# Kernel optimization log

Hardware: AMD Instinct MI355X
Metric: run time of the kernel (lower is better)

Reference implementation:

```python
import jax, jax.numpy as jnp
import numpy as np

N = 50000      # nodes
E = 800000     # edges
DIN = 128      # input feature dim
H = 128        # hidden_channels (cfg.gnn.dim_inner)
DOUT = 64      # output classes
EPS = 1e-5


def setup_inputs() -> dict:
    key = jax.random.key(0)
    ks = jax.random.split(key, 24)
    w = lambda k, s: jax.random.normal(k, s, jnp.float32) * 0.05
    return {
        "x": jax.random.normal(ks[0], (N, DIN), jnp.float32),
        "edge_index": jax.random.randint(ks[1], (2, E), 0, N, jnp.int32),
        # pre-processing 2-layer MLP
        "pre_w1": w(ks[2], (DIN, H)), "pre_b1": jnp.zeros((H,), jnp.float32),
        "pre_w2": w(ks[3], (H, H)),   "pre_b2": jnp.zeros((H,), jnp.float32),
        # 3 GCNConv layers
        "conv_w0": w(ks[4], (H, H)), "conv_b0": jnp.zeros((H,), jnp.float32),
        "conv_w1": w(ks[5], (H, H)), "conv_b1": jnp.zeros((H,), jnp.float32),
        "conv_w2": w(ks[6], (H, H)), "conv_b2": jnp.zeros((H,), jnp.float32),
        # BatchNorm affine params (after conv0 and conv1)
        "bn_g0": jnp.ones((H,), jnp.float32), "bn_b0": jnp.zeros((H,), jnp.float32),
        "bn_g1": jnp.ones((H,), jnp.float32), "bn_b1": jnp.zeros((H,), jnp.float32),
        # post-processing 2-layer MLP
        "post_w1": w(ks[7], (H, H)),    "post_b1": jnp.zeros((H,), jnp.float32),
        "post_w2": w(ks[8], (H, DOUT)), "post_b2": jnp.zeros((DOUT,), jnp.float32),
    }


def _gcn_norm(edge_index):
    # add self loops, compute symmetric normalization D^-1/2 A D^-1/2
    loops = jnp.arange(N, dtype=edge_index.dtype)
    src = jnp.concatenate([edge_index[0], loops])  # [E+N]
    dst = jnp.concatenate([edge_index[1], loops])
    deg = jax.ops.segment_sum(jnp.ones_like(src, jnp.float32), dst, num_segments=N)
    dinv = jnp.where(deg > 0, jax.lax.rsqrt(deg), 0.0)
    norm = dinv[src] * dinv[dst]                   # [E+N]
    return src, dst, norm


def _gcn_conv(x, W, b, src, dst, norm):
    h = x @ W                                      # [N, F_out]
    msg = h[src] * norm[:, None]                   # gather + scale  [E+N, F_out]
    return jax.ops.segment_sum(msg, dst, num_segments=N) + b


def _bn(x, g, b):
    m = x.mean(axis=0)
    v = x.var(axis=0)  # biased, as torch BN uses for normalization
    return (x - m) * jax.lax.rsqrt(v + EPS) * g + b


def reference(x, edge_index, pre_w1, pre_b1, pre_w2, pre_b2,
              conv_w0, conv_b0, conv_w1, conv_b1, conv_w2, conv_b2,
              bn_g0, bn_b0, bn_g1, bn_b1,
              post_w1, post_b1, post_w2, post_b2):
    src, dst, norm = _gcn_norm(edge_index)
    # pre-proc MLP (dropout=0)
    h = jax.nn.relu(x @ pre_w1 + pre_b1)
    h = jax.nn.relu(h @ pre_w2 + pre_b2)
    # conv -> BN -> relu (x2), then final conv
    h = jax.nn.relu(_bn(_gcn_conv(h, conv_w0, conv_b0, src, dst, norm), bn_g0, bn_b0))
    h = jax.nn.relu(_bn(_gcn_conv(h, conv_w1, conv_b1, src, dst, norm), bn_g1, bn_b1))
    h = _gcn_conv(h, conv_w2, conv_b2, src, dst, norm)
    # post-proc MLP
    h = jax.nn.relu(h @ post_w1 + post_b1)
    return h @ post_w2 + post_b2  # [N, DOUT] node logits
```

## Files before the change

kernel.cpp:

```cpp
#include <hip/hip_runtime.h>
#include <hip/hip_bf16.h>

#define NN 50000
#define EE 800000
#define DIN 128
#define HH 128
#define DOUT 64
#define BN_EPS 1e-5f

typedef __attribute__((ext_vector_type(8))) short short8;
typedef __attribute__((ext_vector_type(4))) float floatx4;

static inline size_t align_up(size_t x, size_t a) { return (x + a - 1) & ~(a - 1); }

__device__ __forceinline__ float bf2f(ushort u) {
    uint v = ((uint)u) << 16;
    return __builtin_bit_cast(float, v);
}
__device__ __forceinline__ float bf2f_lo(uint u) { return __builtin_bit_cast(float, u << 16); }
__device__ __forceinline__ float bf2f_hi(uint u) { return __builtin_bit_cast(float, u & 0xffff0000u); }
__device__ __forceinline__ ushort f2bf(float f) {
    uint u = __builtin_bit_cast(uint, f);
    u += 0x7fff + ((u >> 16) & 1);
    return (ushort)(u >> 16);
}
__device__ __forceinline__ uint pack_bf2(float lo, float hi) {
    return (uint)f2bf(lo) | ((uint)f2bf(hi) << 16);
}

__global__ void tcast_all_kernel(const float* __restrict__ s0, const float* __restrict__ s1,
                                 const float* __restrict__ s2, const float* __restrict__ s3,
                                 const float* __restrict__ s4, const float* __restrict__ s5,
                                 const float* __restrict__ s6,
                                 ushort* __restrict__ d0, ushort* __restrict__ d1,
                                 ushort* __restrict__ d2, ushort* __restrict__ d3,
                                 ushort* __restrict__ d4, ushort* __restrict__ d5,
                                 ushort* __restrict__ d6) {
    const float* src; ushort* dst; int F = 128;
    switch (blockIdx.y) {
        case 0: src = s0; dst = d0; break;
        case 1: src = s1; dst = d1; break;
        case 2: src = s2; dst = d2; break;
        case 3: src = s3; dst = d3; break;
        case 4: src = s4; dst = d4; break;
        case 5: src = s5; dst = d5; break;
        default: src = s6; dst = d6; F = 64; break;
    }
    int t = blockIdx.x * 256 + threadIdx.x;
    if (t >= F * 128) return;
    int f = t >> 7, k = t & 127;
    dst[t] = f2bf(src[(size_t)k * F + f]);
}

__global__ void cnt_kernel(const int* __restrict__ ei, int* __restrict__ cnt, int E) {
    int e = (blockIdx.x * 256 + threadIdx.x) * 4;
    if (e + 3 < E) {
        int4 d = *(const int4*)(ei + E + e);
        atomicAdd(&cnt[d.x], 1);
        atomicAdd(&cnt[d.y], 1);
        atomicAdd(&cnt[d.z], 1);
        atomicAdd(&cnt[d.w], 1);
    } else {
        for (; e < E; ++e) atomicAdd(&cnt[ei[E + e]], 1);
    }
}

__device__ __forceinline__ void block_scan256(int v, int* lsum, int& excl, int& total) {
    int lane = threadIdx.x & 63, w = threadIdx.x >> 6;
    int inc = v;
    #pragma unroll
    for (int s = 1; s < 64; s <<= 1) {
        int t = __shfl_up(inc, s);
        if (lane >= s) inc += t;
    }
    if (lane == 63) lsum[w] = inc;
    __syncthreads();
    int pre = 0;
    #pragma unroll
    for (int k = 0; k < 4; ++k)
        if (k < w) pre += lsum[k];
    excl = pre + inc - v;
    total = lsum[0] + lsum[1] + lsum[2] + lsum[3];
    __syncthreads();
}

__global__ void scan_part_kernel(const int* __restrict__ cnt, int* __restrict__ off,
                                 int* __restrict__ bsum, float* __restrict__ dinv, int n) {
    __shared__ int lsum[4];
    int i = blockIdx.x * 256 + threadIdx.x;
    int v = (i < n) ? cnt[i] : 0;
    int excl, total;
    block_scan256(v, lsum, excl, total);
    if (i < n) {
        off[i] = excl;
        dinv[i] = rsqrtf((float)(v + 1));
    }
    if (threadIdx.x == 0) bsum[blockIdx.x] = total;
}

__global__ void scan_bsum_kernel(int* __restrict__ bsum, int nb) {
    __shared__ int lsum[4];
    int t = threadIdx.x;
    int v = (t < nb) ? bsum[t] : 0;
    int excl, total;
    block_scan256(v, lsum, excl, total);
    if (t < nb) bsum[t] = excl;
}

__global__ void scan_add_kernel(int* __restrict__ off, const int* __restrict__ bsum,
                                int* __restrict__ cursor, int n) {
    int i = blockIdx.x * 256 + threadIdx.x;
    if (i < n) {
        int v = off[i] + bsum[blockIdx.x];
        off[i] = v;
        cursor[i] = v;
    }
    if (i == 0) off[n] = EE;
}

__global__ void fill_kernel(const int* __restrict__ ei, int* __restrict__ cursor,
                            int2* __restrict__ csr, const float* __restrict__ dinv, int E) {
    int e = blockIdx.x * 256 + threadIdx.x;
    if (e < E) {
        int s = ei[e];
        int d = ei[E + e];
        int pos = atomicAdd(&cursor[d], 1);
        float w = dinv[s] * dinv[d];
        csr[pos] = make_int2(s, __builtin_bit_cast(int, w));
    }
}

template <int NCG>
__device__ __forceinline__ void zero_acc(floatx4 (&acc)[2][NCG]) {
    #pragma unroll
    for (int rg = 0; rg < 2; ++rg)
        #pragma unroll
        for (int cg = 0; cg < NCG; ++cg)
            acc[rg][cg] = (floatx4){0.f, 0.f, 0.f, 0.f};
}

template <int FO>
__device__ __forceinline__ void stage_w(const ushort* __restrict__ Wt, uint4* Wl, int tid) {
    #pragma unroll
    for (int c = tid; c < FO * 16; c += 256) {
        int f = c >> 4, kb = c & 15;
        Wl[f * 16 + (kb ^ (f & 15))] = ((const uint4*)Wt)[c];
    }
}

template <int NCG>
__device__ __forceinline__ void gemm_step(const uint4* Xl, const uint4* Wl,
                                          floatx4 (&acc)[2][NCG], int wv, int lr, int lk) {
    #pragma unroll
    for (int ks = 0; ks < 4; ++ks) {
        int kb = ks * 4 + lk;
        int swz = kb ^ lr;
        short8 a0 = *(const short8*)&Xl[(wv * 32 + lr) * 16 + swz];
        short8 a1 = *(const short8*)&Xl[(wv * 32 + 16 + lr) * 16 + swz];
        #pragma unroll
        for (int cg = 0; cg < NCG; ++cg) {
            short8 b = *(const short8*)&Wl[(cg * 16 + lr) * 16 + swz];
            acc[0][cg] = __builtin_amdgcn_mfma_f32_16x16x32_bf16(a0, b, acc[0][cg], 0, 0, 0);
            acc[1][cg] = __builtin_amdgcn_mfma_f32_16x16x32_bf16(a1, b, acc[1][cg], 0, 0, 0);
        }
    }
}

template <int NCG>
__device__ __forceinline__ void write_h(floatx4 (&acc)[2][NCG], uint4* Xl,
                                        const float* __restrict__ bias,
                                        int wv, int lr, int lk) {
    ushort* Xs = (ushort*)Xl;
    #pragma unroll
    for (int rg = 0; rg < 2; ++rg)
        #pragma unroll
        for (int cg = 0; cg < NCG; ++cg) {
            int col = cg * 16 + lr;
            float bv = bias[col];
            #pragma unroll
            for (int j = 0; j < 4; ++j) {
                int row = wv * 32 + rg * 16 + lk * 4 + j;
                float o = fmaxf(acc[rg][cg][j] + bv, 0.f);
                Xs[(row * 16 + ((col >> 3) ^ (row & 15))) * 8 + (col & 7)] = f2bf(o);
            }
        }
}

template <int FOUT, bool RELU, bool BIAS, bool OUTF32>
__device__ __forceinline__ void epilogue(floatx4 (&acc)[2][FOUT / 16],
                                         const float* __restrict__ bias, void* Yout,
                                         int row0, int n, int wv, int lr, int lk) {
    #pragma unroll
    for (int rg = 0; rg < 2; ++rg) {
        int rbase = row0 + wv * 32 + rg * 16 + lk * 4;
        #pragma unroll
        for (int cg = 0; cg < FOUT / 16; ++cg) {
            int col = cg * 16 + lr;
            float bv = BIAS ? bias[col] : 0.f;
            #pragma unroll
            for (int j = 0; j < 4; ++j) {
                int r = rbase + j;
                if (r < n) {
                    float o = acc[rg][cg][j] + bv;
                    if (RELU) o = fmaxf(o, 0.f);
                    if (OUTF32)
                        ((float*)Yout)[(size_t)r * FOUT + col] = o;
                    else
                        ((ushort*)Yout)[(size_t)r * FOUT + col] = f2bf(o);
                }
            }
        }
    }
}

__global__ __launch_bounds__(256, 2) void fused_pre_kernel(
    const float* __restrict__ Xg, const ushort* __restrict__ W1t, const float* __restrict__ b1,
    const ushort* __restrict__ W2t, const float* __restrict__ b2,
    const ushort* __restrict__ W3t, ushort* __restrict__ Yout, int n) {
    __shared__ uint4 lds4[4096];
    uint4* Xl = lds4;
    uint4* Wl = lds4 + 2048;
    const int tid = threadIdx.x;
    const int row0 = blockIdx.x * 128;

    for (int c = tid; c < 2048; c += 256) {
        int r = c >> 4, kb = c & 15;
        int row = row0 + r;
        uint4 v = make_uint4(0, 0, 0, 0);
        if (row < n) {
            const float4* p = (const float4*)(Xg + (size_t)row * 128 + kb * 8);
            float4 x0 = p[0], x1 = p[1];
            v.x = pack_bf2(x0.x, x0.y);
            v.y = pack_bf2(x0.z, x0.w);
            v.z = pack_bf2(x1.x, x1.y);
            v.w = pack_bf2(x1.z, x1.w);
        }
        Xl[r * 16 + (kb ^ (r & 15))] = v;
    }
    stage_w<128>(W1t, Wl, tid);
    __syncthreads();

    const int wv = tid >> 6, lane = tid & 63;
    const int lr = lane & 15, lk = lane >> 4;

    floatx4 acc[2][8];
    zero_acc<8>(acc);
    gemm_step<8>(Xl, Wl, acc, wv, lr, lk);
    __syncthreads();
    write_h<8>(acc, Xl, b1, wv, lr, lk);
    stage_w<128>(W2t, Wl, tid);
    __syncthreads();

    zero_acc<8>(acc);
    gemm_step<8>(Xl, Wl, acc, wv, lr, lk);
    __syncthreads();
    write_h<8>(acc, Xl, b2, wv, lr, lk);
    stage_w<128>(W3t, Wl, tid);
    __syncthreads();

    zero_acc<8>(acc);
    gemm_step<8>(Xl, Wl, acc, wv, lr, lk);
    epilogue<128, false, false, false>(acc, nullptr, Yout, row0, n, wv, lr, lk);
}

__global__ __launch_bounds__(256, 2) void fused_post_kernel(
    const ushort* __restrict__ Xg, const ushort* __restrict__ W1t, const float* __restrict__ b1,
    const ushort* __restrict__ W2t, const float* __restrict__ b2,
    float* __restrict__ Yout, int n) {
    __shared__ uint4 lds4[4096];
    uint4* Xl = lds4;
    uint4* Wl = lds4 + 2048;
    const int tid = threadIdx.x;
    const int row0 = blockIdx.x * 128;

    for (int c = tid; c < 2048; c += 256) {
        int r = c >> 4, kb = c & 15;
        int row = row0 + r;
        uint4 v = make_uint4(0, 0, 0, 0);
        if (row < n) v = ((const uint4*)(Xg + (size_t)row * 128))[kb];
        Xl[r * 16 + (kb ^ (r & 15))] = v;
    }
    stage_w<128>(W1t, Wl, tid);
    __syncthreads();

    const int wv = tid >> 6, lane = tid & 63;
    const int lr = lane & 15, lk = lane >> 4;

    floatx4 acc[2][8];
    zero_acc<8>(acc);
    gemm_step<8>(Xl, Wl, acc, wv, lr, lk);
    __syncthreads();
    write_h<8>(acc, Xl, b1, wv, lr, lk);
    stage_w<64>(W2t, Wl, tid);
    __syncthreads();

    floatx4 acc2[2][4];
    zero_acc<4>(acc2);
    gemm_step<4>(Xl, Wl, acc2, wv, lr, lk);
    epilogue<64, false, true, true>(acc2, b2, Yout, row0, n, wv, lr, lk);
}

__global__ __launch_bounds__(256, 2) void gemm_bnf_kernel(
    const ushort* __restrict__ Xg, const ushort* __restrict__ Wt,
    const float* __restrict__ sums, const float* __restrict__ sumsq,
    const float* __restrict__ g, const float* __restrict__ bb,
    ushort* __restrict__ Yout, int n) {
    __shared__ uint4 lds4[4096];
    __shared__ float scf[128], shf[128];
    uint4* Xl = lds4;
    uint4* Wl = lds4 + 2048;
    const int tid = threadIdx.x;
    const int row0 = blockIdx.x * 128;

    if (tid < 128) {
        const float inv_n = 1.0f / (float)NN;
        float m = sums[tid] * inv_n;
        float var = sumsq[tid] * inv_n - m * m;
        float sc = g[tid] * rsqrtf(var + BN_EPS);
        scf[tid] = sc;
        shf[tid] = bb[tid] - m * sc;
    }
    stage_w<128>(Wt, Wl, tid);
    __syncthreads();

    for (int c = tid; c < 2048; c += 256) {
        int r = c >> 4, kb = c & 15;
        int row = row0 + r;
        uint4 v = make_uint4(0, 0, 0, 0);
        if (row < n) v = ((const uint4*)(Xg + (size_t)row * 128))[kb];
        uint a[4] = {v.x, v.y, v.z, v.w};
        #pragma unroll
        for (int p = 0; p < 4; ++p) {
            int f0 = kb * 8 + p * 2;
            float lo = fmaxf(fmaf(bf2f_lo(a[p]), scf[f0], shf[f0]), 0.f);
            float hi = fmaxf(fmaf(bf2f_hi(a[p]), scf[f0 + 1], shf[f0 + 1]), 0.f);
            a[p] = pack_bf2(lo, hi);
        }
        Xl[r * 16 + (kb ^ (r & 15))] = make_uint4(a[0], a[1], a[2], a[3]);
    }
    __syncthreads();

    const int wv = tid >> 6, lane = tid & 63;
    const int lr = lane & 15, lk = lane >> 4;

    floatx4 acc[2][8];
    zero_acc<8>(acc);
    gemm_step<8>(Xl, Wl, acc, wv, lr, lk);
    epilogue<128, false, false, false>(acc, nullptr, Yout, row0, n, wv, lr, lk);
}

__global__ __launch_bounds__(256) void agg16_kernel(const ushort* __restrict__ h,
                                                    const float* __restrict__ dinv,
                                                    const int* __restrict__ off,
                                                    const int2* __restrict__ csr,
                                                    const float* __restrict__ bias,
                                                    ushort* __restrict__ out, int n) {
    int i = (blockIdx.x * 256 + threadIdx.x) >> 6;
    if (i >= n) return;
    int lane = threadIdx.x & 63;

    float di = dinv[i];
    float sw = di * di;
    uint u = ((const uint*)(h + (size_t)i * 128))[lane];
    float a0 = bf2f_lo(u) * sw, a1 = bf2f_hi(u) * sw;

    const int s0 = off[i], s1 = off[i + 1];
    int j = s0;
    for (; j + 4 <= s1; j += 4) {
        int2 ea = csr[j + 0], eb = csr[j + 1];
        int2 ec = csr[j + 2], ed = csr[j + 3];
        float wa = __builtin_bit_cast(float, ea.y), wb = __builtin_bit_cast(float, eb.y);
        float wc = __builtin_bit_cast(float, ec.y), wd = __builtin_bit_cast(float, ed.y);
        uint ua = ((const uint*)(h + (size_t)ea.x * 128))[lane];
        uint ub = ((const uint*)(h + (size_t)eb.x * 128))[lane];
        uint uc = ((const uint*)(h + (size_t)ec.x * 128))[lane];
        uint ud = ((const uint*)(h + (size_t)ed.x * 128))[lane];
        a0 += bf2f_lo(ua) * wa + bf2f_lo(ub) * wb + bf2f_lo(uc) * wc + bf2f_lo(ud) * wd;
        a1 += bf2f_hi(ua) * wa + bf2f_hi(ub) * wb + bf2f_hi(uc) * wc + bf2f_hi(ud) * wd;
    }
    for (; j < s1; ++j) {
        int2 e = csr[j];
        float w = __builtin_bit_cast(float, e.y);
        uint uv = ((const uint*)(h + (size_t)e.x * 128))[lane];
        a0 += bf2f_lo(uv) * w;
        a1 += bf2f_hi(uv) * w;
    }

    float2 b2 = ((const float2*)bias)[lane];
    a0 += b2.x; a1 += b2.y;
    ((uint*)(out + (size_t)i * 128))[lane] = pack_bf2(a0, a1);
}

__global__ __launch_bounds__(256) void bn_stats16_kernel(const ushort* __restrict__ x,
                                                         float* __restrict__ sums,
                                                         float* __restrict__ sumsq, int n) {
    __shared__ float ls[128], lq[128];
    int tid = threadIdx.x;
    if (tid < 128) { ls[tid] = 0.f; lq[tid] = 0.f; }
    __syncthreads();
    int fg = tid & 15, rg = tid >> 4;
    float s[8] = {}, q[8] = {};
    for (int r = blockIdx.x * 16 + rg; r < n; r += gridDim.x * 16) {
        uint4 v = ((const uint4*)(x + (size_t)r * 128))[fg];
        uint a[4] = {v.x, v.y, v.z, v.w};
        #pragma unroll
        for (int p = 0; p < 4; ++p) {
            float lo = bf2f_lo(a[p]), hi = bf2f_hi(a[p]);
            s[2 * p] += lo;     q[2 * p] += lo * lo;
            s[2 * p + 1] += hi; q[2 * p + 1] += hi * hi;
        }
    }
    #pragma unroll
    for (int k = 0; k < 8; ++k) {
        atomicAdd(&ls[fg * 8 + k], s[k]);
        atomicAdd(&lq[fg * 8 + k], q[k]);
    }
    __syncthreads();
    if (tid < 128) {
        atomicAdd(&sums[tid], ls[tid]);
        atomicAdd(&sumsq[tid], lq[tid]);
    }
}

extern "C" void kernel_launch(void* const* d_in, const int* in_sizes, int n_in,
                              void* d_out, int out_size, void* d_ws, size_t ws_size,
                              hipStream_t stream) {
    const float* x        = (const float*)d_in[0];
    const int*   ei       = (const int*)d_in[1];
    const float* pre_w1   = (const float*)d_in[2];
    const float* pre_b1   = (const float*)d_in[3];
    const float* pre_w2   = (const float*)d_in[4];
    const float* pre_b2   = (const float*)d_in[5];
    const float* conv_w0  = (const float*)d_in[6];
    const float* conv_b0  = (const float*)d_in[7];
    const float* conv_w1  = (const float*)d_in[8];
    const float* conv_b1  = (const float*)d_in[9];
    const float* conv_w2  = (const float*)d_in[10];
    const float* conv_b2  = (const float*)d_in[11];
    const float* bn_g0    = (const float*)d_in[12];
    const float* bn_b0    = (const float*)d_in[13];
    const float* bn_g1    = (const float*)d_in[14];
    const float* bn_b1    = (const float*)d_in[15];
    const float* post_w1  = (const float*)d_in[16];
    const float* post_b1  = (const float*)d_in[17];
    const float* post_w2  = (const float*)d_in[18];
    const float* post_b2  = (const float*)d_in[19];
    float* out = (float*)d_out;

    const int n = NN, E = EE;
    const int NB = (n + 255) / 256;

    char* w = (char*)d_ws;
    int* cnt    = (int*)w;   w += (size_t)n * 4;
    float* bns0 = (float*)w;
    float* bnq0 = bns0 + 128;
    float* bns1 = bns0 + 256;
    float* bnq1 = bns0 + 384;
    w += align_up(512 * 4, 512);
    int* cursor = (int*)w;   w += align_up((size_t)n * 4, 512);
    int* bsum   = (int*)w;   w += align_up(256 * 4, 512);
    int* off    = (int*)w;   w += align_up((size_t)(n + 1) * 4, 512);
    float* dinv = (float*)w; w += align_up((size_t)n * 4, 512);
    int2* csr   = (int2*)w;  w += align_up((size_t)E * 8, 512);
    ushort* wt_pre1  = (ushort*)w; w += align_up(128 * 128 * 2, 512);
    ushort* wt_pre2  = (ushort*)w; w += align_up(128 * 128 * 2, 512);
    ushort* wt_c0    = (ushort*)w; w += align_up(128 * 128 * 2, 512);
    ushort* wt_c1    = (ushort*)w; w += align_up(128 * 128 * 2, 512);
    ushort* wt_c2    = (ushort*)w; w += align_up(128 * 128 * 2, 512);
    ushort* wt_post1 = (ushort*)w; w += align_up(128 * 128 * 2, 512);
    ushort* wt_post2 = (ushort*)w; w += align_up(64 * 128 * 2, 512);
    ushort* P = (ushort*)w; w += align_up((size_t)n * 128 * 2, 512);
    ushort* Q = (ushort*)w; w += align_up((size_t)n * 128 * 2, 512);
    ushort* R = (ushort*)w; w += align_up((size_t)n * 128 * 2, 512);

    hipMemsetAsync(cnt, 0, (size_t)n * 4 + 512 * 4, stream);

    tcast_all_kernel<<<dim3(64, 7), 256, 0, stream>>>(
        pre_w1, pre_w2, conv_w0, conv_w1, conv_w2, post_w1, post_w2,
        wt_pre1, wt_pre2, wt_c0, wt_c1, wt_c2, wt_post1, wt_post2);

    cnt_kernel<<<(E / 4 + 255) / 256, 256, 0, stream>>>(ei, cnt, E);
    scan_part_kernel<<<NB, 256, 0, stream>>>(cnt, off, bsum, dinv, n);
    scan_bsum_kernel<<<1, 256, 0, stream>>>(bsum, NB);
    scan_add_kernel<<<NB, 256, 0, stream>>>(off, bsum, cursor, n);
    fill_kernel<<<(E + 255) / 256, 256, 0, stream>>>(ei, cursor, csr, dinv, E);

    const int gb = (n + 127) / 128;
    const int agg_blocks = (n * 64 + 255) / 256;

    fused_pre_kernel<<<gb, 256, 0, stream>>>(x, wt_pre1, pre_b1, wt_pre2, pre_b2, wt_c0, P, n);
    agg16_kernel<<<agg_blocks, 256, 0, stream>>>(P, dinv, off, csr, conv_b0, Q, n);
    bn_stats16_kernel<<<256, 256, 0, stream>>>(Q, bns0, bnq0, n);

    gemm_bnf_kernel<<<gb, 256, 0, stream>>>(Q, wt_c1, bns0, bnq0, bn_g0, bn_b0, P, n);
    agg16_kernel<<<agg_blocks, 256, 0, stream>>>(P, dinv, off, csr, conv_b1, R, n);
    bn_stats16_kernel<<<256, 256, 0, stream>>>(R, bns1, bnq1, n);

    gemm_bnf_kernel<<<gb, 256, 0, stream>>>(R, wt_c2, bns1, bnq1, bn_g1, bn_b1, P, n);
    agg16_kernel<<<agg_blocks, 256, 0, stream>>>(P, dinv, off, csr, conv_b2, Q, n);

    fused_post_kernel<<<gb, 256, 0, stream>>>(Q, wt_post1, post_b1, wt_post2, post_b2, out, n);
}
```

Before: 408.8 us.

## Split GCN aggregation into feature quarters and store only source indices in CSR

The aggregation kernel now splits the 128 features into four 32-feature quarters, each handled by a separate block range. Within a quarter, each 16-lane group processes one node, and all blocks for a quarter are scheduled together. The aim is to keep that quarter's slice of the feature table resident in L2/LLC while the random neighbor gathers run. The CSR now stores only the source index, shrinking it from 8 to 4 bytes per edge; the edge weight is recomputed as dinv[src]*dinv[dst] inside the kernel. In exchange, each edge's index is read four times and needs an extra random dinv gather, and each gather fetches only 64 bytes per row.

```diff
diff --git a/kernel.cpp b/kernel.cpp
--- a/kernel.cpp
+++ b/kernel.cpp
@@ -119,14 +119,13 @@
 }
 
 __global__ void fill_kernel(const int* __restrict__ ei, int* __restrict__ cursor,
-                            int2* __restrict__ csr, const float* __restrict__ dinv, int E) {
+                            int* __restrict__ csr, int E) {
     int e = blockIdx.x * 256 + threadIdx.x;
     if (e < E) {
         int s = ei[e];
         int d = ei[E + e];
         int pos = atomicAdd(&cursor[d], 1);
-        float w = dinv[s] * dinv[d];
-        csr[pos] = make_int2(s, __builtin_bit_cast(int, w));
+        csr[pos] = s;
     }
 }
 
@@ -349,46 +348,52 @@
     epilogue<128, false, false, false>(acc, nullptr, Yout, row0, n, wv, lr, lk);
 }
 
-__global__ __launch_bounds__(256) void agg16_kernel(const ushort* __restrict__ h,
-                                                    const float* __restrict__ dinv,
-                                                    const int* __restrict__ off,
-                                                    const int2* __restrict__ csr,
-                                                    const float* __restrict__ bias,
-                                                    ushort* __restrict__ out, int n) {
-    int i = (blockIdx.x * 256 + threadIdx.x) >> 6;
-    if (i >= n) return;
-    int lane = threadIdx.x & 63;
-
-    float di = dinv[i];
+#define AGG_CPQ (NN / 16)
+__global__ __launch_bounds__(256) void aggq_kernel(const ushort* __restrict__ h,
+                                                   const float* __restrict__ dinv,
+                                                   const int* __restrict__ off,
+                                                   const int* __restrict__ csr,
+                                                   const float* __restrict__ bias,
+                                                   ushort* __restrict__ out) {
+    const int q = blockIdx.x / AGG_CPQ;
+    const int c = blockIdx.x % AGG_CPQ;
+    const int tid = threadIdx.x;
+    const int wv = tid >> 6, l = tid & 63;
+    const int g = l >> 4, l16 = l & 15;
+    const int node = c * 16 + wv * 4 + g;
+    const int base = q * 16 + l16;
+
+    const uint* __restrict__ hq = (const uint*)h;
+    float di = dinv[node];
+    uint u = hq[(size_t)node * 64 + base];
     float sw = di * di;
-    uint u = ((const uint*)(h + (size_t)i * 128))[lane];
     float a0 = bf2f_lo(u) * sw, a1 = bf2f_hi(u) * sw;
 
-    const int s0 = off[i], s1 = off[i + 1];
+    const int s0 = off[node], s1 = off[node + 1];
     int j = s0;
     for (; j + 4 <= s1; j += 4) {
-        int2 ea = csr[j + 0], eb = csr[j + 1];
-        int2 ec = csr[j + 2], ed = csr[j + 3];
-        float wa = __builtin_bit_cast(float, ea.y), wb = __builtin_bit_cast(float, eb.y);
-        float wc = __builtin_bit_cast(float, ec.y), wd = __builtin_bit_cast(float, ed.y);
-        uint ua = ((const uint*)(h + (size_t)ea.x * 128))[lane];
-        uint ub = ((const uint*)(h + (size_t)eb.x * 128))[lane];
-        uint uc = ((const uint*)(h + (size_t)ec.x * 128))[lane];
-        uint ud = ((const uint*)(h + (size_t)ed.x * 128))[lane];
+        int sa = csr[j + 0], sb = csr[j + 1];
+        int sc = csr[j + 2], sd = csr[j + 3];
+        float wa = dinv[sa] * di, wb = dinv[sb] * di;
+        float wc = dinv[sc] * di, wd = dinv[sd] * di;
+        uint ua = hq[(size_t)sa * 64 + base];
+        uint ub = hq[(size_t)sb * 64 + base];
+        uint uc = hq[(size_t)sc * 64 + base];
+        uint ud = hq[(size_t)sd * 64 + base];
         a0 += bf2f_lo(ua) * wa + bf2f_lo(ub) * wb + bf2f_lo(uc) * wc + bf2f_lo(ud) * wd;
         a1 += bf2f_hi(ua) * wa + bf2f_hi(ub) * wb + bf2f_hi(uc) * wc + bf2f_hi(ud) * wd;
     }
     for (; j < s1; ++j) {
-        int2 e = csr[j];
-        float w = __builtin_bit_cast(float, e.y);
-        uint uv = ((const uint*)(h + (size_t)e.x * 128))[lane];
+        int s = csr[j];
+        float w = dinv[s] * di;
+        uint uv = hq[(size_t)s * 64 + base];
         a0 += bf2f_lo(uv) * w;
         a1 += bf2f_hi(uv) * w;
     }
 
-    float2 b2 = ((const float2*)bias)[lane];
+    float2 b2 = ((const float2*)bias)[base];
     a0 += b2.x; a1 += b2.y;
-    ((uint*)(out + (size_t)i * 128))[lane] = pack_bf2(a0, a1);
+    ((uint*)out)[(size_t)node * 64 + base] = pack_bf2(a0, a1);
 }
 
 __global__ __launch_bounds__(256) void bn_stats16_kernel(const ushort* __restrict__ x,
@@ -461,7 +466,7 @@
     int* bsum   = (int*)w;   w += align_up(256 * 4, 512);
     int* off    = (int*)w;   w += align_up((size_t)(n + 1) * 4, 512);
     float* dinv = (float*)w; w += align_up((size_t)n * 4, 512);
-    int2* csr   = (int2*)w;  w += align_up((size_t)E * 8, 512);
+    int* csr    = (int*)w;   w += align_up((size_t)E * 4, 512);
     ushort* wt_pre1  = (ushort*)w; w += align_up(128 * 128 * 2, 512);
     ushort* wt_pre2  = (ushort*)w; w += align_up(128 * 128 * 2, 512);
     ushort* wt_c0    = (ushort*)w; w += align_up(128 * 128 * 2, 512);
@@ -483,21 +488,21 @@
     scan_part_kernel<<<NB, 256, 0, stream>>>(cnt, off, bsum, dinv, n);
     scan_bsum_kernel<<<1, 256, 0, stream>>>(bsum, NB);
     scan_add_kernel<<<NB, 256, 0, stream>>>(off, bsum, cursor, n);
-    fill_kernel<<<(E + 255) / 256, 256, 0, stream>>>(ei, cursor, csr, dinv, E);
+    fill_kernel<<<(E + 255) / 256, 256, 0, stream>>>(ei, cursor, csr, E);
 
     const int gb = (n + 127) / 128;
-    const int agg_blocks = (n * 64 + 255) / 256;
+    const int agg_blocks = 4 * AGG_CPQ;
 
     fused_pre_kernel<<<gb, 256, 0, stream>>>(x, wt_pre1, pre_b1, wt_pre2, pre_b2, wt_c0, P, n);
-    agg16_kernel<<<agg_blocks, 256, 0, stream>>>(P, dinv, off, csr, conv_b0, Q, n);
+    aggq_kernel<<<agg_blocks, 256, 0, stream>>>(P, dinv, off, csr, conv_b0, Q);
     bn_stats16_kernel<<<256, 256, 0, stream>>>(Q, bns0, bnq0, n);
 
     gemm_bnf_kernel<<<gb, 256, 0, stream>>>(Q, wt_c1, bns0, bnq0, bn_g0, bn_b0, P, n);
-    agg16_kernel<<<agg_blocks, 256, 0, stream>>>(P, dinv, off, csr, conv_b1, R, n);
+    aggq_kernel<<<agg_blocks, 256, 0, stream>>>(P, dinv, off, csr, conv_b1, R);
     bn_stats16_kernel<<<256, 256, 0, stream>>>(R, bns1, bnq1, n);
 
     gemm_bnf_kernel<<<gb, 256, 0, stream>>>(R, wt_c2, bns1, bnq1, bn_g1, bn_b1, P, n);
-    agg16_kernel<<<agg_blocks, 256, 0, stream>>>(P, dinv, off, csr, conv_b2, Q, n);
+    aggq_kernel<<<agg_blocks, 256, 0, stream>>>(P, dinv, off, csr, conv_b2, Q);
 
     fused_post_kernel<<<gb, 256, 0, stream>>>(Q, wt_post1, post_b1, wt_post2, post_b2, out, n);
 }
```

After: 452.2 us. 1.11x slower.
